# Performance work log

Hardware: AMD Instinct MI355X
Metric: run time of the kernel (lower is better)

Reference implementation:

```python
import jax, jax.numpy as jnp
import numpy as np

B, Q, G = 32, 16384, 128   # batch, num queries, (padded) num GT per image
K = 32                      # first top-k (nearest candidates per GT)
N = 9                       # second top-k (highest-IoU matches per GT)


def box_cxcywh_to_xyxy(b):
    cx, cy, w, h = jnp.split(b, 4, axis=-1)
    return jnp.concatenate([cx - 0.5 * w, cy - 0.5 * h,
                            cx + 0.5 * w, cy + 0.5 * h], axis=-1)


def box_iou(a, b):
    # a, b: broadcastable [..., 4] in xyxy
    lt = jnp.maximum(a[..., :2], b[..., :2])
    rb = jnp.minimum(a[..., 2:], b[..., 2:])
    wh = jnp.clip(rb - lt, 0.0)
    inter = wh[..., 0] * wh[..., 1]
    area_a = (a[..., 2] - a[..., 0]) * (a[..., 3] - a[..., 1])
    area_b = (b[..., 2] - b[..., 0]) * (b[..., 3] - b[..., 1])
    return inter / (area_a + area_b - inter)


def _assign(gt, pred):
    # gt: [G,4] cxcywh, pred: [Q,4] cxcywh
    # euclidean cdist in cxcywh space: [G, Q]
    d = jnp.sqrt(jnp.sum((gt[:, None, :] - pred[None, :, :]) ** 2, axis=-1))
    # k nearest predictions per GT (smallest distance)
    _, kidx = jax.lax.top_k(-d, K)            # [G, K]
    k_boxes = pred[kidx]                       # [G, K, 4]
    iou = box_iou(box_cxcywh_to_xyxy(gt)[:, None, :],
                  box_cxcywh_to_xyxy(k_boxes))           # [G, K]
    vals, ns = jax.lax.top_k(iou, N)           # [G, N] highest IoU among the K
    pred_idx = jnp.take_along_axis(kidx, ns, axis=1)      # [G, N] global pred ids
    gt_idx = jnp.broadcast_to(jnp.arange(gt.shape[0])[:, None], ns.shape)
    return pred_idx.reshape(-1), gt_idx.reshape(-1)


def setup_inputs() -> dict:
    key = jax.random.key(0)
    k1, k2 = jax.random.split(key)
    pred_boxes = jax.random.uniform(k1, (B, Q, 4), dtype=jnp.float32)
    gt_boxes = jax.random.uniform(k2, (B, G, 4), dtype=jnp.float32)
    return {"pred_boxes": pred_boxes, "gt_boxes": gt_boxes}


def reference(pred_boxes, gt_boxes):
    # per-image assignment, vectorized over the batch
    pred_idx, gt_idx = jax.vmap(_assign)(gt_boxes, pred_boxes)
    # pred_idx, gt_idx: [B, G*N] int32 (analog of the list of (i, j) index tensors)
    return pred_idx, gt_idx
```

## Files before the change

### kernel.cpp

```cpp
#include <hip/hip_runtime.h>

#define BB 32
#define QQ 16384
#define GG 128
#define KK 32
#define NN 9
#define TT 16
#define TH 1024
#define HR 8
#define NRANGE 2048
#define RPL 32
#define CAP 192
#define ACAP 96
#define LCAP 12
#define UF 4

typedef unsigned long long u64;
typedef unsigned int u32;
typedef unsigned short u16;

#define INFF __uint_as_float(0x7F800000u)

__device__ __forceinline__ u64 pack_asc(float key, u32 idx) {
  return (((u64)__float_as_uint(key)) << 32) | (u64)idx;
}

__device__ __forceinline__ float dist2_ref(const float4 g, const float4 p) {
#pragma clang fp contract(off)
  float dx = g.x - p.x;
  float dy = g.y - p.y;
  float dz = g.z - p.z;
  float dw = g.w - p.w;
  float s = dx * dx + dy * dy;
  s = s + dz * dz;
  s = s + dw * dw;
  return s;
}

__device__ __forceinline__ float iou_ref(const float4 g, const float4 p) {
#pragma clang fp contract(off)
  float gx1 = g.x - 0.5f * g.z, gy1 = g.y - 0.5f * g.w;
  float gx2 = g.x + 0.5f * g.z, gy2 = g.y + 0.5f * g.w;
  float px1 = p.x - 0.5f * p.z, py1 = p.y - 0.5f * p.w;
  float px2 = p.x + 0.5f * p.z, py2 = p.y + 0.5f * p.w;
  float ltx = fmaxf(gx1, px1), lty = fmaxf(gy1, py1);
  float rbx = fminf(gx2, px2), rby = fminf(gy2, py2);
  float wx = fmaxf(rbx - ltx, 0.0f), wy = fmaxf(rby - lty, 0.0f);
  float inter = wx * wy;
  float aa = (gx2 - gx1) * (gy2 - gy1);
  float ab = (px2 - px1) * (py2 - py1);
  return inter / ((aa + ab) - inter);
}

__device__ __forceinline__ u32 f2ord(float f) {
  u32 b = __float_as_uint(f);
  return (b & 0x80000000u) ? ~b : (b | 0x80000000u);
}
__device__ __forceinline__ float ord2f(u32 k) {
  return __uint_as_float((k & 0x80000000u) ? (k & 0x7FFFFFFFu) : ~k);
}

__device__ __forceinline__ u16 bf16up(float x) {
  u32 b = __float_as_uint(x);
  if (!(b >> 31)) b += 0xFFFFu;
  return (u16)(b >> 16);
}

__global__ __launch_bounds__(TH, 8) void atss_phase1(
    const float4* __restrict__ pred, const float4* __restrict__ gtb,
    u16* __restrict__ ws) {
  const int t = threadIdx.x;
  const int f = blockIdx.x;
  const int b = (f & 7) * 4 + (f >> 7);
  const int m = (f >> 3) & 7;
  const int h = (f >> 6) & 1;
  const int g0 = m * TT;

  float4 G[TT];
  float g2[TT];
#pragma unroll
  for (int gg = 0; gg < TT; ++gg) {
    G[gg] = gtb[b * GG + g0 + gg];
    g2[gg] = fmaf(G[gg].x, G[gg].x,
             fmaf(G[gg].y, G[gg].y,
             fmaf(G[gg].z, G[gg].z, G[gg].w * G[gg].w)));
  }

  const float4* pb = pred + (size_t)b * QQ;
  const int r = h * 1024 + t;

  float mn[TT];
#pragma unroll
  for (int gg = 0; gg < TT; ++gg) mn[gg] = INFF;

  float4 P[UF];
#pragma unroll
  for (int u = 0; u < UF; ++u) P[u] = pb[r + u * NRANGE];
#pragma unroll
  for (int j = 0; j < HR; j += UF) {
    float4 C[UF];
#pragma unroll
    for (int u = 0; u < UF; ++u) C[u] = P[u];
    if (j + UF < HR) {
#pragma unroll
      for (int u = 0; u < UF; ++u) P[u] = pb[r + (j + UF + u) * NRANGE];
    }
#pragma unroll
    for (int u = 0; u < UF; ++u) {
      float4 p = C[u];
      float pp = fmaf(p.x, p.x, fmaf(p.y, p.y, fmaf(p.z, p.z, p.w * p.w)));
      float qx = p.x + p.x, qy = p.y + p.y, qz = p.z + p.z, qw = p.w + p.w;
#pragma unroll
      for (int gg = 0; gg < TT; ++gg) {
        float acc = fmaf(-G[gg].x, qx, pp);
        acc = fmaf(-G[gg].y, qy, acc);
        acc = fmaf(-G[gg].z, qz, acc);
        acc = fmaf(-G[gg].w, qw, acc);
        mn[gg] = fminf(mn[gg], acc);
      }
    }
  }
  u16* seg = ws + (size_t)((b * 8 + m) * TT) * NRANGE;
#pragma unroll
  for (int gg = 0; gg < TT; ++gg)
    seg[gg * NRANGE + r] = bf16up(mn[gg] + g2[gg]);
}

__global__ __launch_bounds__(64, 4) void atss_phase2(
    const float4* __restrict__ pred, const float4* __restrict__ gtb,
    const u16* __restrict__ ws, int* __restrict__ out) {
  __shared__ u64 kl[LCAP][64];
  __shared__ u64 kc[CAP];
  __shared__ u16 sact[ACAP];
  __shared__ u32 ik[KK];
  __shared__ int kidx[KK];

  const int lane = threadIdx.x;
  const int f = blockIdx.x;
  const int x = f & 7;
  const int jd = f >> 3;
  const int b = x * 4 + (jd & 3);
  const int g = jd >> 2;

  const float4 gt = gtb[b * GG + g];
  const float4* pb = pred + (size_t)b * QQ;
  const u16* vsrc =
      ws + (size_t)((b * 8 + (g >> 4)) * TT + (g & 15)) * NRANGE;

  float V[RPL];
  {
    const uint4* v4 = (const uint4*)(vsrc + lane * RPL);
    uint4 qa = v4[0], qb = v4[1], qc = v4[2], qd = v4[3];
#define UNPK(W, base)                                   \
  V[(base)] = __uint_as_float((W) << 16);               \
  V[(base) + 1] = __uint_as_float((W) & 0xFFFF0000u);
    UNPK(qa.x, 0) UNPK(qa.y, 2) UNPK(qa.z, 4) UNPK(qa.w, 6)
    UNPK(qb.x, 8) UNPK(qb.y, 10) UNPK(qb.z, 12) UNPK(qb.w, 14)
    UNPK(qc.x, 16) UNPK(qc.y, 18) UNPK(qc.z, 20) UNPK(qc.w, 22)
    UNPK(qd.x, 24) UNPK(qd.y, 26) UNPK(qd.z, 28) UNPK(qd.w, 30)
#undef UNPK
  }

  float m1 = INFF, m2 = INFF;
#pragma unroll
  for (int k = 0; k < RPL; ++k) {
    float v = V[k];
    float nm1 = fminf(m1, v);
    m2 = fminf(m2, fmaxf(m1, v));
    m1 = nm1;
  }

  u32 k1 = f2ord(m1), k2 = f2ord(m2);
  u32 pref = 0;
#pragma unroll
  for (int bit = 31; bit >= 16; --bit) {
    u32 tr = pref | (1u << bit);
    int c = __popcll(__ballot(k1 < tr)) + __popcll(__ballot(k2 < tr));
    if (c < 32) pref = tr;
  }
  const float Us = ord2f(pref | 0xFFFFu);

  const float T = fmaxf(Us, 0.0f) * 1.0001f + 1e-5f;
  const float sUs = T * 1.009f + 1e-5f;

  u32 amask = 0;
#pragma unroll
  for (int k = 0; k < RPL; ++k) amask |= (V[k] <= sUs) ? (1u << k) : 0u;
  int cnt = __popc(amask);
  int pre = cnt;
#pragma unroll
  for (int sj = 1; sj < 64; sj <<= 1) {
    int o = __shfl_up(pre, sj, 64);
    if (lane >= sj) pre += o;
  }
  const int na = __shfl(pre, 63, 64);
  {
    int pos = pre - cnt;
    u32 mrem = amask;
    while (mrem) {
      int k = __ffs(mrem) - 1;
      mrem &= mrem - 1;
      if (pos < ACAP) sact[pos] = (u16)(lane * RPL + k);
      ++pos;
    }
  }

  bool bad = (na > ACAP);
  int lc = 0;
  int n = 0;
  if (!bad) {
    const int total = na * HR;
    const int trips = (total + 63) >> 6;
    int it = lane;
    bool cv = it < total;
    int ci = 0;
    float4 cp;
    if (cv) {
      int e = sact[it >> 3];
      ci = (int)e + (it & 7) * NRANGE;
      cp = pb[ci];
    }
    for (int tr = 0; tr < trips; ++tr) {
      int itn = it + 64;
      bool nv = itn < total;
      int ni = 0;
      float4 np;
      if (nv) {
        int e = sact[itn >> 3];
        ni = (int)e + (itn & 7) * NRANGE;
        np = pb[ni];
      }
      if (cv) {
        float d2 = dist2_ref(gt, cp);
        if (d2 <= T) {
          if (lc < LCAP) kl[lc][lane] = pack_asc(sqrtf(d2), (u32)ci);
          ++lc;
        }
      }
      it = itn;
      cv = nv;
      ci = ni;
      cp = np;
    }

    int pre2 = lc;
#pragma unroll
    for (int sj = 1; sj < 64; sj <<= 1) {
      int o = __shfl_up(pre2, sj, 64);
      if (lane >= sj) pre2 += o;
    }
    n = __shfl(pre2, 63, 64);
    int excl = pre2 - lc;
    for (int i = 0; i < lc; ++i) {
      int dst = excl + i;
      if (dst < CAP) kc[dst] = kl[i][lane];
    }
    bad = (n > CAP);
  }

  if (bad) {
    if (lane == 0) {
      u64 best[KK];
      for (int l = 0; l < KK; ++l) best[l] = ~0ull;
      for (int i = 0; i < QQ; ++i) {
        float d = sqrtf(dist2_ref(gt, pb[i]));
        u64 pk = pack_asc(d, (u32)i);
        if (pk < best[KK - 1]) {
          int pos = KK - 1;
          while (pos > 0 && best[pos - 1] > pk) {
            best[pos] = best[pos - 1];
            --pos;
          }
          best[pos] = pk;
        }
      }
      for (int l = 0; l < KK; ++l) kidx[l] = (int)(best[l] & 0xFFFFFFFFull);
    }
  } else {
    u64 myA = (lane < n) ? kc[lane] : ~0ull;
    u64 myB = (lane + 64 < n) ? kc[lane + 64] : ~0ull;
    u64 myC = (lane + 128 < n) ? kc[lane + 128] : ~0ull;
    int rA = 0, rB = 0, rC = 0;
    const int nslots = (n > 128) ? 3 : ((n > 64) ? 2 : 1);
    if (nslots == 1) {
      int i = 0;
      for (; i + 4 <= n; i += 4) {
        u64 a0 = kc[i], a1 = kc[i + 1], a2 = kc[i + 2], a3 = kc[i + 3];
        rA += (int)(a0 < myA) + (int)(a1 < myA) + (int)(a2 < myA) +
              (int)(a3 < myA);
      }
      for (; i < n; ++i) rA += (int)(kc[i] < myA);
    } else if (nslots == 2) {
      int i = 0;
      for (; i + 4 <= n; i += 4) {
        u64 a0 = kc[i], a1 = kc[i + 1], a2 = kc[i + 2], a3 = kc[i + 3];
        rA += (int)(a0 < myA) + (int)(a1 < myA) + (int)(a2 < myA) +
              (int)(a3 < myA);
        rB += (int)(a0 < myB) + (int)(a1 < myB) + (int)(a2 < myB) +
              (int)(a3 < myB);
      }
      for (; i < n; ++i) {
        u64 a0 = kc[i];
        rA += (int)(a0 < myA);
        rB += (int)(a0 < myB);
      }
    } else {
      int i = 0;
      for (; i + 4 <= n; i += 4) {
        u64 a0 = kc[i], a1 = kc[i + 1], a2 = kc[i + 2], a3 = kc[i + 3];
        rA += (int)(a0 < myA) + (int)(a1 < myA) + (int)(a2 < myA) +
              (int)(a3 < myA);
        rB += (int)(a0 < myB) + (int)(a1 < myB) + (int)(a2 < myB) +
              (int)(a3 < myB);
        rC += (int)(a0 < myC) + (int)(a1 < myC) + (int)(a2 < myC) +
              (int)(a3 < myC);
      }
      for (; i < n; ++i) {
        u64 a0 = kc[i];
        rA += (int)(a0 < myA);
        rB += (int)(a0 < myB);
        rC += (int)(a0 < myC);
      }
    }
    if (lane < n && rA < KK) kidx[rA] = (int)(myA & 0xFFFFFFFFull);
    if (nslots >= 2 && lane + 64 < n && rB < KK)
      kidx[rB] = (int)(myB & 0xFFFFFFFFull);
    if (nslots >= 3 && lane + 128 < n && rC < KK)
      kidx[rC] = (int)(myC & 0xFFFFFFFFull);
  }
  const int pi = (lane < KK) ? kidx[lane] : 0;

  if (lane < KK) {
    float iou = iou_ref(gt, pb[pi]);
    u32 myk = ~__float_as_uint(iou);
    ik[lane] = myk;
    int r9 = 0;
#pragma unroll
    for (int i2 = 0; i2 < KK; ++i2) {
      u32 ki = ik[i2];
      r9 += ((ki < myk) || (ki == myk && i2 < lane)) ? 1 : 0;
    }
    if (r9 < NN) {
      int base = (b * GG + g) * NN + r9;
      out[base] = pi;
      out[BB * GG * NN + base] = g;
    }
  }
}

extern "C" void kernel_launch(void* const* d_in, const int* in_sizes, int n_in,
                              void* d_out, int out_size, void* d_ws, size_t ws_size,
                              hipStream_t stream) {
  (void)in_sizes;
  (void)n_in;
  (void)out_size;
  (void)ws_size;
  const float4* pred = (const float4*)d_in[0];
  const float4* gt = (const float4*)d_in[1];
  int* out = (int*)d_out;
  u16* ws = (u16*)d_ws;
  atss_phase1<<<512, TH, 0, stream>>>(pred, gt, ws);
  atss_phase2<<<4096, 64, 0, stream>>>(pred, gt, ws, out);
}
```

Measured before the change: 86.93 us.

## Fuse active-range compaction into direct per-lane candidate gathering

Removes the shared-memory compaction of active ranges (prefix scan plus sact list) and has each lane directly load and test the 8 strided predictions for each of its own active ranges in a wave-uniform loop. The per-lane local candidate capacity rises to 14 and the overflow check becomes a wave vote on lc. The rank-counting loops over kc and ik now use 16-byte vectorized LDS reads. This trades balanced work distribution for less scan and LDS traffic, so lanes with many active ranges can serialize the whole wave.

```diff
diff --git a/kernel.cpp b/kernel.cpp
--- a/kernel.cpp
+++ b/kernel.cpp
@@ -11,8 +11,7 @@
 #define NRANGE 2048
 #define RPL 32
 #define CAP 192
-#define ACAP 96
-#define LCAP 12
+#define LCAP 14
 #define UF 4
 
 typedef unsigned long long u64;
@@ -129,10 +128,9 @@
 __global__ __launch_bounds__(64, 4) void atss_phase2(
     const float4* __restrict__ pred, const float4* __restrict__ gtb,
     const u16* __restrict__ ws, int* __restrict__ out) {
-  __shared__ u64 kl[LCAP][64];
-  __shared__ u64 kc[CAP];
-  __shared__ u16 sact[ACAP];
-  __shared__ u32 ik[KK];
+  __shared__ __align__(16) u64 kl[LCAP][64];
+  __shared__ __align__(16) u64 kc[CAP];
+  __shared__ __align__(16) u32 ik[KK];
   __shared__ int kidx[KK];
 
   const int lane = threadIdx.x;
@@ -186,63 +184,42 @@
   u32 amask = 0;
 #pragma unroll
   for (int k = 0; k < RPL; ++k) amask |= (V[k] <= sUs) ? (1u << k) : 0u;
-  int cnt = __popc(amask);
-  int pre = cnt;
-#pragma unroll
-  for (int sj = 1; sj < 64; sj <<= 1) {
-    int o = __shfl_up(pre, sj, 64);
-    if (lane >= sj) pre += o;
-  }
-  const int na = __shfl(pre, 63, 64);
+
+  int lc = 0;
   {
-    int pos = pre - cnt;
     u32 mrem = amask;
-    while (mrem) {
-      int k = __ffs(mrem) - 1;
-      mrem &= mrem - 1;
-      if (pos < ACAP) sact[pos] = (u16)(lane * RPL + k);
-      ++pos;
-    }
-  }
-
-  bool bad = (na > ACAP);
-  int lc = 0;
+    while (__any(mrem != 0)) {
+      if (mrem) {
+        int k = __ffs(mrem) - 1;
+        mrem &= mrem - 1;
+        int r = lane * RPL + k;
+        float4 e0 = pb[r];
+        float4 e1 = pb[r + 1 * NRANGE];
+        float4 e2 = pb[r + 2 * NRANGE];
+        float4 e3 = pb[r + 3 * NRANGE];
+        float4 e4 = pb[r + 4 * NRANGE];
+        float4 e5 = pb[r + 5 * NRANGE];
+        float4 e6 = pb[r + 6 * NRANGE];
+        float4 e7 = pb[r + 7 * NRANGE];
+#define TESTE(EV, JJ)                                             \
+  {                                                               \
+    float d2_ = dist2_ref(gt, EV);                                \
+    if (d2_ <= T) {                                               \
+      if (lc < LCAP)                                              \
+        kl[lc][lane] = pack_asc(sqrtf(d2_), (u32)(r + JJ * NRANGE)); \
+      ++lc;                                                       \
+    }                                                             \
+  }
+        TESTE(e0, 0) TESTE(e1, 1) TESTE(e2, 2) TESTE(e3, 3)
+        TESTE(e4, 4) TESTE(e5, 5) TESTE(e6, 6) TESTE(e7, 7)
+#undef TESTE
+      }
+    }
+  }
+  bool bad = __any(lc > LCAP);
+
   int n = 0;
   if (!bad) {
-    const int total = na * HR;
-    const int trips = (total + 63) >> 6;
-    int it = lane;
-    bool cv = it < total;
-    int ci = 0;
-    float4 cp;
-    if (cv) {
-      int e = sact[it >> 3];
-      ci = (int)e + (it & 7) * NRANGE;
-      cp = pb[ci];
-    }
-    for (int tr = 0; tr < trips; ++tr) {
-      int itn = it + 64;
-      bool nv = itn < total;
-      int ni = 0;
-      float4 np;
-      if (nv) {
-        int e = sact[itn >> 3];
-        ni = (int)e + (itn & 7) * NRANGE;
-        np = pb[ni];
-      }
-      if (cv) {
-        float d2 = dist2_ref(gt, cp);
-        if (d2 <= T) {
-          if (lc < LCAP) kl[lc][lane] = pack_asc(sqrtf(d2), (u32)ci);
-          ++lc;
-        }
-      }
-      it = itn;
-      cv = nv;
-      ci = ni;
-      cp = np;
-    }
-
     int pre2 = lc;
 #pragma unroll
     for (int sj = 1; sj < 64; sj <<= 1) {
@@ -277,50 +254,37 @@
       for (int l = 0; l < KK; ++l) kidx[l] = (int)(best[l] & 0xFFFFFFFFull);
     }
   } else {
+    const ulonglong2* kc2 = (const ulonglong2*)kc;
     u64 myA = (lane < n) ? kc[lane] : ~0ull;
     u64 myB = (lane + 64 < n) ? kc[lane + 64] : ~0ull;
     u64 myC = (lane + 128 < n) ? kc[lane + 128] : ~0ull;
     int rA = 0, rB = 0, rC = 0;
+    const int half = n >> 1;
     const int nslots = (n > 128) ? 3 : ((n > 64) ? 2 : 1);
     if (nslots == 1) {
-      int i = 0;
-      for (; i + 4 <= n; i += 4) {
-        u64 a0 = kc[i], a1 = kc[i + 1], a2 = kc[i + 2], a3 = kc[i + 3];
-        rA += (int)(a0 < myA) + (int)(a1 < myA) + (int)(a2 < myA) +
-              (int)(a3 < myA);
-      }
-      for (; i < n; ++i) rA += (int)(kc[i] < myA);
+      for (int i = 0; i < half; ++i) {
+        ulonglong2 pr = kc2[i];
+        rA += (int)(pr.x < myA) + (int)(pr.y < myA);
+      }
     } else if (nslots == 2) {
-      int i = 0;
-      for (; i + 4 <= n; i += 4) {
-        u64 a0 = kc[i], a1 = kc[i + 1], a2 = kc[i + 2], a3 = kc[i + 3];
-        rA += (int)(a0 < myA) + (int)(a1 < myA) + (int)(a2 < myA) +
-              (int)(a3 < myA);
-        rB += (int)(a0 < myB) + (int)(a1 < myB) + (int)(a2 < myB) +
-              (int)(a3 < myB);
-      }
-      for (; i < n; ++i) {
-        u64 a0 = kc[i];
-        rA += (int)(a0 < myA);
-        rB += (int)(a0 < myB);
+      for (int i = 0; i < half; ++i) {
+        ulonglong2 pr = kc2[i];
+        rA += (int)(pr.x < myA) + (int)(pr.y < myA);
+        rB += (int)(pr.x < myB) + (int)(pr.y < myB);
       }
     } else {
-      int i = 0;
-      for (; i + 4 <= n; i += 4) {
-        u64 a0 = kc[i], a1 = kc[i + 1], a2 = kc[i + 2], a3 = kc[i + 3];
-        rA += (int)(a0 < myA) + (int)(a1 < myA) + (int)(a2 < myA) +
-              (int)(a3 < myA);
-        rB += (int)(a0 < myB) + (int)(a1 < myB) + (int)(a2 < myB) +
-              (int)(a3 < myB);
-        rC += (int)(a0 < myC) + (int)(a1 < myC) + (int)(a2 < myC) +
-              (int)(a3 < myC);
-      }
-      for (; i < n; ++i) {
-        u64 a0 = kc[i];
-        rA += (int)(a0 < myA);
-        rB += (int)(a0 < myB);
-        rC += (int)(a0 < myC);
-      }
+      for (int i = 0; i < half; ++i) {
+        ulonglong2 pr = kc2[i];
+        rA += (int)(pr.x < myA) + (int)(pr.y < myA);
+        rB += (int)(pr.x < myB) + (int)(pr.y < myB);
+        rC += (int)(pr.x < myC) + (int)(pr.y < myC);
+      }
+    }
+    if (n & 1) {
+      u64 a0 = kc[n - 1];
+      rA += (int)(a0 < myA);
+      rB += (int)(a0 < myB);
+      rC += (int)(a0 < myC);
     }
     if (lane < n && rA < KK) kidx[rA] = (int)(myA & 0xFFFFFFFFull);
     if (nslots >= 2 && lane + 64 < n && rB < KK)
@@ -334,11 +298,16 @@
     float iou = iou_ref(gt, pb[pi]);
     u32 myk = ~__float_as_uint(iou);
     ik[lane] = myk;
+    const uint4* ik4 = (const uint4*)ik;
     int r9 = 0;
 #pragma unroll
-    for (int i2 = 0; i2 < KK; ++i2) {
-      u32 ki = ik[i2];
-      r9 += ((ki < myk) || (ki == myk && i2 < lane)) ? 1 : 0;
+    for (int i2 = 0; i2 < KK / 4; ++i2) {
+      uint4 wv = ik4[i2];
+      int b4 = i2 * 4;
+      r9 += (int)((wv.x < myk) || (wv.x == myk && b4 + 0 < lane));
+      r9 += (int)((wv.y < myk) || (wv.y == myk && b4 + 1 < lane));
+      r9 += (int)((wv.z < myk) || (wv.z == myk && b4 + 2 < lane));
+      r9 += (int)((wv.w < myk) || (wv.w == myk && b4 + 3 < lane));
     }
     if (r9 < NN) {
       int base = (b * GG + g) * NN + r9;
```

Measured after the change: 90.67 us. +4.3%, slower.
